# Kernel tuning notes

Measured on AMD Instinct MI355X. Metric: run time of the kernel, lower is better.

The kernel has to match this reference:

```python
import jax, jax.numpy as jnp
import numpy as np

BAND_WIDTH = 0.05
EPS = 1e-5
NORM_EPS = 1e-12  # F.normalize clamp_min


def _l2_normalize_channels(x):
    # x: (B, C, D, H, W); normalize over channel dim=1 like F.normalize(p=2, dim=1)
    n = jnp.sqrt(jnp.sum(x * x, axis=1, keepdims=True))
    return x / jnp.maximum(n, NORM_EPS)


def setup_inputs() -> dict:
    key = jax.random.key(0)
    k1, k2, k3 = jax.random.split(key, 3)
    B, C, D, H, W = 2, 256, 8, 8, 8
    P, K = 128, 512  # n_patches iterations, k=512 sampled voxels per patch
    S = D * H * W  # 512 spatial voxels
    t2_feat = jax.random.normal(k1, (B, C, D, H, W), dtype=jnp.float32)
    t1_feat = jax.random.normal(k2, (B, C, D, H, W), dtype=jnp.float32)
    idx = jax.random.randint(k3, (P, K), 0, S, dtype=jnp.int32)
    return {"t2_feat": t2_feat, "t1_feat": t1_feat, "idx": idx}


def reference(t2_feat, t1_feat, idx):
    B, C = t2_feat.shape[:2]
    # normalize channels, flatten spatial dims: (B, C, S)
    t2 = _l2_normalize_channels(t2_feat).reshape(B, C, -1)
    t1 = _l2_normalize_channels(t1_feat).reshape(B, C, -1)
    # gather the same random voxels for both modalities: (B, C, P, K)
    t2p = t2[:, :, idx]
    t1p = t1[:, :, idx]
    # batched cosine similarity: bmm(t2p^T, t1p) per patch -> (P, B, K, K)
    cs = jnp.einsum('bcpk,bcpl->pbkl', t2p, t1p)
    e = jnp.exp(cs / BAND_WIDTH)
    pos = jnp.diagonal(e, axis1=2, axis2=3)  # (P, B, K) exp of positives
    # InfoNCE over columns (torch dim=1 of (B,K,K)) and rows (dim=2)
    info_nce1 = pos / jnp.sum(e, axis=2)
    info_nce2 = pos / jnp.sum(e, axis=3)
    info_nce = 0.5 * (info_nce1 + info_nce2)
    # per-patch mean of -log, then mean over patches == global mean
    return jnp.mean(-jnp.log(info_nce + EPS))
```

## Files before the change

### kernel.cpp

```cpp
#include <hip/hip_runtime.h>

typedef __attribute__((ext_vector_type(8))) short bf16x8;
typedef __attribute__((ext_vector_type(4))) float f32x4;
typedef __attribute__((ext_vector_type(4))) ushort u16x4;

#define C_DIM 256
#define S_DIM 512
#define P_DIM 128
#define K_DIM 512
#define INV_BW 20.0f
#define EPS_LOSS 1e-5f

#define OFF_SS2    0
#define OFF_SS1    1024
#define OFF_DIAG   2048
#define OFF_CNTBF  3072
#define OFF_T2BF   35840
#define OFF_T1BF   166912
#define OFF_EBF    297984
#define OFF_ETBF   560128
#define OFF_D1     822272
#define OFF_D2     1084416
#define OFF_PART   1346560
#define OFF_BAR    1346816

__device__ inline ushort f2bf(float f) {
  union { float f; uint u; } v; v.f = f;
  return (ushort)((v.u + 0x7FFF + ((v.u >> 16) & 1)) >> 16);
}

#define TP 260
__global__ __launch_bounds__(256) void pre_kernel(
    const float* __restrict__ t2, const float* __restrict__ t1,
    const int* __restrict__ idx,
    float* __restrict__ ss2, float* __restrict__ ss1,
    ushort* __restrict__ t2bfT, ushort* __restrict__ t1bfT,
    ushort* __restrict__ cntbf, int* __restrict__ bar) {
  int blk = blockIdx.x, tid = threadIdx.x;
  if (blk < 128) {
    __shared__ ushort tl[16][TP];
    __shared__ float ps[16][17];
    int tt = blk >> 6, b = (blk >> 5) & 1, stile = blk & 31;
    int s0 = stile * 16;
    const float* src = (tt ? t1 : t2) + b * (C_DIM * S_DIM);
    ushort* dst = (tt ? t1bfT : t2bfT) + b * (S_DIM * C_DIM);
    float* ssd = (tt ? ss1 : ss2) + b * S_DIM;
    int ls = tid & 15, cg = tid >> 4;
    float a = 0.f;
    #pragma unroll
    for (int k = 0; k < 16; ++k) {
      int c = cg + 16 * k;
      float v = src[c * S_DIM + s0 + ls];
      a += v * v;
      tl[ls][c] = f2bf(v);
    }
    ps[cg][ls] = a;
    __syncthreads();
    if (tid < 16) {
      float ss = 0.f;
      #pragma unroll
      for (int j = 0; j < 16; ++j) ss += ps[j][tid];
      ssd[s0 + tid] = ss;
    }
    int wv = tid >> 6, ln = tid & 63;
    #pragma unroll
    for (int i = 0; i < 4; ++i) {
      int sl = wv * 4 + i;
      u16x4 pk = *reinterpret_cast<const u16x4*>(&tl[sl][ln * 4]);
      *reinterpret_cast<u16x4*>(&dst[(s0 + sl) * C_DIM + ln * 4]) = pk;
    }
  } else {
    __shared__ int c_lds[S_DIM];
    int p = blk - 128;
    if (blk == 128 && tid < 3) bar[tid] = 0;
    c_lds[tid] = 0; c_lds[tid + 256] = 0;
    __syncthreads();
    atomicAdd(&c_lds[idx[p * K_DIM + tid]], 1);
    atomicAdd(&c_lds[idx[p * K_DIM + tid + 256]], 1);
    __syncthreads();
    cntbf[p * S_DIM + tid]       = f2bf((float)c_lds[tid]);
    cntbf[p * S_DIM + tid + 256] = f2bf((float)c_lds[tid + 256]);
  }
}

__global__ __launch_bounds__(256) void gemm_exp_mfma_kernel(
    const ushort* __restrict__ t2bfT, const ushort* __restrict__ t1bfT,
    const float* __restrict__ ss2, const float* __restrict__ ss1,
    ushort* __restrict__ Ebf, ushort* __restrict__ ETbf,
    float* __restrict__ diag) {
  int wave = threadIdx.x >> 6, lane = threadIdx.x & 63;
  int job = blockIdx.x * 4 + wave;
  int n = job & 31, mp = (job >> 5) & 15, b = job >> 9;
  int c0 = n * 16;
  int lr = lane & 15, lo = lane >> 4;
  const ushort* base2 = t2bfT + b * (S_DIM * C_DIM);
  const ushort* bp = t1bfT + b * (S_DIM * C_DIM) + (c0 + lr) * C_DIM + lo * 8;
  bf16x8 bfr[8];
  #pragma unroll
  for (int k = 0; k < 8; ++k)
    bfr[k] = *reinterpret_cast<const bf16x8*>(bp + k * 32);
  float bs = 1.0f / fmaxf(sqrtf(ss1[b * S_DIM + c0 + lr]), 1e-12f);
  ushort* Eb  = Ebf  + b * (S_DIM * S_DIM);
  ushort* ETb = ETbf + b * (S_DIM * S_DIM);
  #pragma unroll
  for (int t = 0; t < 2; ++t) {
    int m0 = mp * 32 + t * 16;
    const ushort* ap = base2 + (m0 + lr) * C_DIM + lo * 8;
    f32x4 acc = {0.f, 0.f, 0.f, 0.f};
    #pragma unroll
    for (int k = 0; k < 8; ++k) {
      bf16x8 af = *reinterpret_cast<const bf16x8*>(ap + k * 32);
      acc = __builtin_amdgcn_mfma_f32_16x16x32_bf16(af, bfr[k], acc, 0, 0, 0);
    }
    float e[4]; ushort eb[4];
    #pragma unroll
    for (int r = 0; r < 4; ++r) {
      int row = m0 + lo * 4 + r;
      float as = 1.0f / fmaxf(sqrtf(ss2[b * S_DIM + row]), 1e-12f);
      e[r] = __expf(acc[r] * as * bs * INV_BW);
      eb[r] = f2bf(e[r]);
      Eb[row * S_DIM + c0 + lr] = eb[r];
    }
    u16x4 pk = {eb[0], eb[1], eb[2], eb[3]};
    *reinterpret_cast<u16x4*>(&ETb[(c0 + lr) * S_DIM + m0 + lo * 4]) = pk;
    if (m0 == c0 && (lr >> 2) == lo) diag[b * S_DIM + m0 + lr] = e[lr & 3];
  }
}

__global__ __launch_bounds__(256) void denom_mfma_kernel(
    const ushort* __restrict__ Ebf, const ushort* __restrict__ ETbf,
    const ushort* __restrict__ cntbf,
    float* __restrict__ D1, float* __restrict__ D2) {
  int wave = threadIdx.x >> 6, lane = threadIdx.x & 63;
  int job = blockIdx.x * 4 + wave;
  int np = job & 15, m = (job >> 4) & 7, b = (job >> 7) & 1;
  int z = (job >> 8) & 1, h = job >> 9;
  int m0 = m * 16;
  int lr = lane & 15, lo = lane >> 4;
  const ushort* Bmat = (z ? Ebf : ETbf) + b * (S_DIM * S_DIM);
  float* Dp = (z ? D2 : D1);
  const ushort* aptr = cntbf + (m0 + lr) * S_DIM + h * 256 + lo * 8;
  bf16x8 afr[8];
  #pragma unroll
  for (int k = 0; k < 8; ++k)
    afr[k] = *reinterpret_cast<const bf16x8*>(aptr + k * 32);
  #pragma unroll
  for (int t = 0; t < 2; ++t) {
    int col0 = np * 32 + t * 16;
    const ushort* bptr = Bmat + (col0 + lr) * S_DIM + h * 256 + lo * 8;
    f32x4 acc = {0.f, 0.f, 0.f, 0.f};
    #pragma unroll
    for (int k = 0; k < 8; ++k) {
      bf16x8 bv = *reinterpret_cast<const bf16x8*>(bptr + k * 32);
      acc = __builtin_amdgcn_mfma_f32_16x16x32_bf16(afr[k], bv, acc, 0, 0, 0);
    }
    #pragma unroll
    for (int r = 0; r < 4; ++r) {
      int p = m0 + lo * 4 + r;
      Dp[((h * P_DIM + p) * 2 + b) * S_DIM + col0 + lr] = acc[r];
    }
  }
}

__global__ __launch_bounds__(512) void loss_final_kernel(
    const int* __restrict__ idx, const float* __restrict__ diag,
    const float* __restrict__ D1, const float* __restrict__ D2,
    float* __restrict__ part, int* __restrict__ bar, float* __restrict__ out) {
  const int HOFF = P_DIM * 2 * S_DIM;
  int p = blockIdx.x, k = threadIdx.x;
  int s = idx[p * K_DIM + k];
  float acc = 0.f;
  #pragma unroll
  for (int b = 0; b < 2; ++b) {
    float pos = diag[b * S_DIM + s];
    int o = (p * 2 + b) * S_DIM + s;
    float d1 = D1[o] + D1[HOFF + o];
    float d2 = D2[o] + D2[HOFF + o];
    acc += __logf(0.5f * (pos / d1 + pos / d2) + EPS_LOSS);
  }
  for (int o = 32; o; o >>= 1) acc += __shfl_down(acc, o);
  __shared__ float red[8];
  __shared__ int lastflag;
  if ((k & 63) == 0) red[k >> 6] = acc;
  __syncthreads();
  if (k == 0) {
    float tsum = 0.f;
    #pragma unroll
    for (int i = 0; i < 8; ++i) tsum += red[i];
    atomicExch(&part[p], tsum);
    __threadfence();
    int old = atomicAdd(&bar[2], 1);
    lastflag = (old == P_DIM - 1);
  }
  __syncthreads();
  if (lastflag) {
    __threadfence();
    float v = (k < P_DIM) ? atomicAdd(&part[k], 0.0f) : 0.0f;
    for (int o = 32; o; o >>= 1) v += __shfl_down(v, o);
    __shared__ float red2[8];
    if ((k & 63) == 0) red2[k >> 6] = v;
    __syncthreads();
    if (k == 0) {
      float tsum = 0.f;
      #pragma unroll
      for (int i = 0; i < 8; ++i) tsum += red2[i];
      out[0] = -tsum * (1.0f / (P_DIM * 2.0f * K_DIM));
    }
  }
}

extern "C" void kernel_launch(void* const* d_in, const int* in_sizes, int n_in,
                              void* d_out, int out_size, void* d_ws, size_t ws_size,
                              hipStream_t stream) {
  const float* t2 = (const float*)d_in[0];
  const float* t1 = (const float*)d_in[1];
  const int* idx  = (const int*)d_in[2];
  float* ws = (float*)d_ws;
  float*  ss2    = ws + OFF_SS2;
  float*  ss1    = ws + OFF_SS1;
  float*  diag   = ws + OFF_DIAG;
  ushort* cntbf  = (ushort*)(ws + OFF_CNTBF);
  ushort* t2bfT  = (ushort*)(ws + OFF_T2BF);
  ushort* t1bfT  = (ushort*)(ws + OFF_T1BF);
  ushort* Ebf    = (ushort*)(ws + OFF_EBF);
  ushort* ETbf   = (ushort*)(ws + OFF_ETBF);
  float*  D1     = ws + OFF_D1;
  float*  D2     = ws + OFF_D2;
  float*  part   = ws + OFF_PART;
  int*    bar    = (int*)(ws + OFF_BAR);

  pre_kernel<<<256, 256, 0, stream>>>(t2, t1, idx, ss2, ss1, t2bfT, t1bfT,
                                      cntbf, bar);
  gemm_exp_mfma_kernel<<<256, 256, 0, stream>>>(t2bfT, t1bfT, ss2, ss1,
                                                Ebf, ETbf, diag);
  denom_mfma_kernel<<<256, 256, 0, stream>>>(Ebf, ETbf, cntbf, D1, D2);
  loss_final_kernel<<<P_DIM, 512, 0, stream>>>(idx, diag, D1, D2, part, bar,
                                               (float*)d_out);
}
```

Before: 30.08 us.

## Fuse preprocessing into gram-exp and histogram kernels, drop a launch

Removes the separate preprocessing kernel. The gram/exp kernel now loads fp32 features directly, converts them to bf16 in LDS and computes channel norms locally. Each 32x32 tile re-reads its input slice, which adds redundant global reads in exchange for one fewer launch and no transposed intermediate buffers. The denominator kernel builds per-patch voxel histograms in LDS from idx and runs the full K=512 reduction per block, so the split-K halves and their summation in the loss kernel go away. The catch is that every block recomputes its histograms, duplicating that atomic work.

```diff
diff --git a/kernel.cpp b/kernel.cpp
--- a/kernel.cpp
+++ b/kernel.cpp
@@ -11,154 +11,133 @@
 #define INV_BW 20.0f
 #define EPS_LOSS 1e-5f
 
-#define OFF_SS2    0
-#define OFF_SS1    1024
-#define OFF_DIAG   2048
-#define OFF_CNTBF  3072
-#define OFF_T2BF   35840
-#define OFF_T1BF   166912
-#define OFF_EBF    297984
-#define OFF_ETBF   560128
-#define OFF_D1     822272
-#define OFF_D2     1084416
-#define OFF_PART   1346560
-#define OFF_BAR    1346816
+#define OFF_DIAG   0
+#define OFF_EBF    1024
+#define OFF_ETBF   263168
+#define OFF_D1     525312
+#define OFF_D2     656384
+#define OFF_PART   787456
+#define OFF_BAR    787584
 
 __device__ inline ushort f2bf(float f) {
   union { float f; uint u; } v; v.f = f;
   return (ushort)((v.u + 0x7FFF + ((v.u >> 16) & 1)) >> 16);
 }
-
-#define TP 260
-__global__ __launch_bounds__(256) void pre_kernel(
+__device__ inline float bf2f(ushort u) {
+  union { uint u; float f; } v; v.u = ((uint)u) << 16;
+  return v.f;
+}
+
+__global__ __launch_bounds__(256) void gram_exp_kernel(
     const float* __restrict__ t2, const float* __restrict__ t1,
-    const int* __restrict__ idx,
-    float* __restrict__ ss2, float* __restrict__ ss1,
-    ushort* __restrict__ t2bfT, ushort* __restrict__ t1bfT,
-    ushort* __restrict__ cntbf, int* __restrict__ bar) {
+    ushort* __restrict__ Ebf, ushort* __restrict__ ETbf,
+    float* __restrict__ diag, int* __restrict__ bar) {
+  __shared__ ushort A_[32][264];
+  __shared__ ushort B_[32][264];
+  __shared__ float sA[32], sB[32];
   int blk = blockIdx.x, tid = threadIdx.x;
-  if (blk < 128) {
-    __shared__ ushort tl[16][TP];
-    __shared__ float ps[16][17];
-    int tt = blk >> 6, b = (blk >> 5) & 1, stile = blk & 31;
-    int s0 = stile * 16;
-    const float* src = (tt ? t1 : t2) + b * (C_DIM * S_DIM);
-    ushort* dst = (tt ? t1bfT : t2bfT) + b * (S_DIM * C_DIM);
-    float* ssd = (tt ? ss1 : ss2) + b * S_DIM;
-    int ls = tid & 15, cg = tid >> 4;
-    float a = 0.f;
-    #pragma unroll
-    for (int k = 0; k < 16; ++k) {
-      int c = cg + 16 * k;
-      float v = src[c * S_DIM + s0 + ls];
-      a += v * v;
-      tl[ls][c] = f2bf(v);
-    }
-    ps[cg][ls] = a;
-    __syncthreads();
-    if (tid < 16) {
-      float ss = 0.f;
-      #pragma unroll
-      for (int j = 0; j < 16; ++j) ss += ps[j][tid];
-      ssd[s0 + tid] = ss;
-    }
-    int wv = tid >> 6, ln = tid & 63;
-    #pragma unroll
-    for (int i = 0; i < 4; ++i) {
-      int sl = wv * 4 + i;
-      u16x4 pk = *reinterpret_cast<const u16x4*>(&tl[sl][ln * 4]);
-      *reinterpret_cast<u16x4*>(&dst[(s0 + sl) * C_DIM + ln * 4]) = pk;
-    }
-  } else {
-    __shared__ int c_lds[S_DIM];
-    int p = blk - 128;
-    if (blk == 128 && tid < 3) bar[tid] = 0;
-    c_lds[tid] = 0; c_lds[tid + 256] = 0;
-    __syncthreads();
-    atomicAdd(&c_lds[idx[p * K_DIM + tid]], 1);
-    atomicAdd(&c_lds[idx[p * K_DIM + tid + 256]], 1);
-    __syncthreads();
-    cntbf[p * S_DIM + tid]       = f2bf((float)c_lds[tid]);
-    cntbf[p * S_DIM + tid + 256] = f2bf((float)c_lds[tid + 256]);
-  }
-}
-
-__global__ __launch_bounds__(256) void gemm_exp_mfma_kernel(
-    const ushort* __restrict__ t2bfT, const ushort* __restrict__ t1bfT,
-    const float* __restrict__ ss2, const float* __restrict__ ss1,
-    ushort* __restrict__ Ebf, ushort* __restrict__ ETbf,
-    float* __restrict__ diag) {
-  int wave = threadIdx.x >> 6, lane = threadIdx.x & 63;
-  int job = blockIdx.x * 4 + wave;
-  int n = job & 31, mp = (job >> 5) & 15, b = job >> 9;
-  int c0 = n * 16;
+  if (blk == 0 && tid == 0) bar[0] = 0;
+  int mb = blk & 15, nb = (blk >> 4) & 15, b = blk >> 8;
+  int m0 = mb * 32, c0 = nb * 32;
+  {
+    const float* pa = t2 + (b * C_DIM + tid) * S_DIM + m0;
+    const float* pb = t1 + (b * C_DIM + tid) * S_DIM + c0;
+    #pragma unroll
+    for (int q = 0; q < 8; ++q) {
+      float4 va = *reinterpret_cast<const float4*>(pa + q * 4);
+      float4 vb = *reinterpret_cast<const float4*>(pb + q * 4);
+      A_[q * 4 + 0][tid] = f2bf(va.x); A_[q * 4 + 1][tid] = f2bf(va.y);
+      A_[q * 4 + 2][tid] = f2bf(va.z); A_[q * 4 + 3][tid] = f2bf(va.w);
+      B_[q * 4 + 0][tid] = f2bf(vb.x); B_[q * 4 + 1][tid] = f2bf(vb.y);
+      B_[q * 4 + 2][tid] = f2bf(vb.z); B_[q * 4 + 3][tid] = f2bf(vb.w);
+    }
+  }
+  __syncthreads();
+  if (tid < 64) {
+    const ushort* row = (tid < 32) ? &A_[tid][0] : &B_[tid - 32][0];
+    float a0 = 0.f, a1 = 0.f, a2 = 0.f, a3 = 0.f;
+    #pragma unroll
+    for (int k = 0; k < 64; ++k) {
+      u16x4 v = *reinterpret_cast<const u16x4*>(row + k * 4);
+      float x0 = bf2f(v.x), x1 = bf2f(v.y), x2 = bf2f(v.z), x3 = bf2f(v.w);
+      a0 += x0 * x0; a1 += x1 * x1; a2 += x2 * x2; a3 += x3 * x3;
+    }
+    float sc = 1.0f / fmaxf(sqrtf((a0 + a1) + (a2 + a3)), 1e-12f);
+    if (tid < 32) sA[tid] = sc; else sB[tid - 32] = sc;
+  }
+  __syncthreads();
+  int wave = tid >> 6, lane = tid & 63;
+  int tm = wave & 1, tn = wave >> 1;
   int lr = lane & 15, lo = lane >> 4;
-  const ushort* base2 = t2bfT + b * (S_DIM * C_DIM);
-  const ushort* bp = t1bfT + b * (S_DIM * C_DIM) + (c0 + lr) * C_DIM + lo * 8;
-  bf16x8 bfr[8];
-  #pragma unroll
-  for (int k = 0; k < 8; ++k)
-    bfr[k] = *reinterpret_cast<const bf16x8*>(bp + k * 32);
-  float bs = 1.0f / fmaxf(sqrtf(ss1[b * S_DIM + c0 + lr]), 1e-12f);
+  f32x4 acc = {0.f, 0.f, 0.f, 0.f};
+  #pragma unroll
+  for (int k = 0; k < 8; ++k) {
+    bf16x8 af = *reinterpret_cast<const bf16x8*>(&A_[tm * 16 + lr][lo * 8 + k * 32]);
+    bf16x8 bv = *reinterpret_cast<const bf16x8*>(&B_[tn * 16 + lr][lo * 8 + k * 32]);
+    acc = __builtin_amdgcn_mfma_f32_16x16x32_bf16(af, bv, acc, 0, 0, 0);
+  }
+  int mg0 = m0 + tm * 16, cg0 = c0 + tn * 16;
+  float bs = sB[tn * 16 + lr];
   ushort* Eb  = Ebf  + b * (S_DIM * S_DIM);
   ushort* ETb = ETbf + b * (S_DIM * S_DIM);
-  #pragma unroll
-  for (int t = 0; t < 2; ++t) {
-    int m0 = mp * 32 + t * 16;
-    const ushort* ap = base2 + (m0 + lr) * C_DIM + lo * 8;
-    f32x4 acc = {0.f, 0.f, 0.f, 0.f};
-    #pragma unroll
-    for (int k = 0; k < 8; ++k) {
-      bf16x8 af = *reinterpret_cast<const bf16x8*>(ap + k * 32);
-      acc = __builtin_amdgcn_mfma_f32_16x16x32_bf16(af, bfr[k], acc, 0, 0, 0);
-    }
-    float e[4]; ushort eb[4];
-    #pragma unroll
-    for (int r = 0; r < 4; ++r) {
-      int row = m0 + lo * 4 + r;
-      float as = 1.0f / fmaxf(sqrtf(ss2[b * S_DIM + row]), 1e-12f);
-      e[r] = __expf(acc[r] * as * bs * INV_BW);
-      eb[r] = f2bf(e[r]);
-      Eb[row * S_DIM + c0 + lr] = eb[r];
-    }
-    u16x4 pk = {eb[0], eb[1], eb[2], eb[3]};
-    *reinterpret_cast<u16x4*>(&ETb[(c0 + lr) * S_DIM + m0 + lo * 4]) = pk;
-    if (m0 == c0 && (lr >> 2) == lo) diag[b * S_DIM + m0 + lr] = e[lr & 3];
-  }
-}
-
-__global__ __launch_bounds__(256) void denom_mfma_kernel(
+  float e[4]; ushort eb[4];
+  #pragma unroll
+  for (int r = 0; r < 4; ++r) {
+    int rl = tm * 16 + lo * 4 + r;
+    float ev = __expf(acc[r] * sA[rl] * bs * INV_BW);
+    e[r] = ev; eb[r] = f2bf(ev);
+    Eb[(m0 + rl) * S_DIM + cg0 + lr] = eb[r];
+  }
+  u16x4 pk = {eb[0], eb[1], eb[2], eb[3]};
+  *reinterpret_cast<u16x4*>(&ETb[(cg0 + lr) * S_DIM + mg0 + lo * 4]) = pk;
+  if (mg0 == cg0 && (lr >> 2) == lo) diag[b * S_DIM + mg0 + lr] = e[lr & 3];
+}
+
+__global__ __launch_bounds__(256) void denom_kernel(
     const ushort* __restrict__ Ebf, const ushort* __restrict__ ETbf,
-    const ushort* __restrict__ cntbf,
+    const int* __restrict__ idx,
     float* __restrict__ D1, float* __restrict__ D2) {
-  int wave = threadIdx.x >> 6, lane = threadIdx.x & 63;
-  int job = blockIdx.x * 4 + wave;
-  int np = job & 15, m = (job >> 4) & 7, b = (job >> 7) & 1;
-  int z = (job >> 8) & 1, h = job >> 9;
-  int m0 = m * 16;
+  __shared__ int hist[16][516];
+  __shared__ ushort cb[16][520];
+  int blk = blockIdx.x, tid = threadIdx.x;
+  int m = blk & 7, ng = (blk >> 3) & 7, b = (blk >> 6) & 1, z = blk >> 7;
+  int p0 = m * 16;
+  #pragma unroll
+  for (int i = 0; i < 32; ++i) hist[(tid * 32 + i) >> 9][(tid * 32 + i) & 511] = 0;
+  __syncthreads();
+  {
+    int p = tid >> 4, l16 = tid & 15;
+    const int* ip = idx + (p0 + p) * K_DIM + l16;
+    #pragma unroll
+    for (int j = 0; j < 32; ++j) atomicAdd(&hist[p][ip[j * 16]], 1);
+  }
+  __syncthreads();
+  {
+    int p = tid >> 4, l16 = tid & 15;
+    #pragma unroll
+    for (int j = 0; j < 32; ++j) {
+      int col = l16 + j * 16;
+      cb[p][col] = f2bf((float)hist[p][col]);
+    }
+  }
+  __syncthreads();
+  int wave = tid >> 6, lane = tid & 63;
   int lr = lane & 15, lo = lane >> 4;
+  int col0 = (ng * 4 + wave) * 16;
   const ushort* Bmat = (z ? Ebf : ETbf) + b * (S_DIM * S_DIM);
-  float* Dp = (z ? D2 : D1);
-  const ushort* aptr = cntbf + (m0 + lr) * S_DIM + h * 256 + lo * 8;
-  bf16x8 afr[8];
-  #pragma unroll
-  for (int k = 0; k < 8; ++k)
-    afr[k] = *reinterpret_cast<const bf16x8*>(aptr + k * 32);
-  #pragma unroll
-  for (int t = 0; t < 2; ++t) {
-    int col0 = np * 32 + t * 16;
-    const ushort* bptr = Bmat + (col0 + lr) * S_DIM + h * 256 + lo * 8;
-    f32x4 acc = {0.f, 0.f, 0.f, 0.f};
-    #pragma unroll
-    for (int k = 0; k < 8; ++k) {
-      bf16x8 bv = *reinterpret_cast<const bf16x8*>(bptr + k * 32);
-      acc = __builtin_amdgcn_mfma_f32_16x16x32_bf16(afr[k], bv, acc, 0, 0, 0);
-    }
-    #pragma unroll
-    for (int r = 0; r < 4; ++r) {
-      int p = m0 + lo * 4 + r;
-      Dp[((h * P_DIM + p) * 2 + b) * S_DIM + col0 + lr] = acc[r];
-    }
+  const ushort* bptr = Bmat + (col0 + lr) * S_DIM + lo * 8;
+  f32x4 acc = {0.f, 0.f, 0.f, 0.f};
+  #pragma unroll
+  for (int k = 0; k < 16; ++k) {
+    bf16x8 af = *reinterpret_cast<const bf16x8*>(&cb[lr][lo * 8 + k * 32]);
+    bf16x8 bv = *reinterpret_cast<const bf16x8*>(bptr + k * 32);
+    acc = __builtin_amdgcn_mfma_f32_16x16x32_bf16(af, bv, acc, 0, 0, 0);
+  }
+  float* Dp = z ? D2 : D1;
+  #pragma unroll
+  for (int r = 0; r < 4; ++r) {
+    int p = p0 + lo * 4 + r;
+    Dp[(p * 2 + b) * S_DIM + col0 + lr] = acc[r];
   }
 }
 
@@ -166,7 +145,6 @@
     const int* __restrict__ idx, const float* __restrict__ diag,
     const float* __restrict__ D1, const float* __restrict__ D2,
     float* __restrict__ part, int* __restrict__ bar, float* __restrict__ out) {
-  const int HOFF = P_DIM * 2 * S_DIM;
   int p = blockIdx.x, k = threadIdx.x;
   int s = idx[p * K_DIM + k];
   float acc = 0.f;
@@ -174,8 +152,8 @@
   for (int b = 0; b < 2; ++b) {
     float pos = diag[b * S_DIM + s];
     int o = (p * 2 + b) * S_DIM + s;
-    float d1 = D1[o] + D1[HOFF + o];
-    float d2 = D2[o] + D2[HOFF + o];
+    float d1 = D1[o];
+    float d2 = D2[o];
     acc += __logf(0.5f * (pos / d1 + pos / d2) + EPS_LOSS);
   }
   for (int o = 32; o; o >>= 1) acc += __shfl_down(acc, o);
@@ -189,7 +167,7 @@
     for (int i = 0; i < 8; ++i) tsum += red[i];
     atomicExch(&part[p], tsum);
     __threadfence();
-    int old = atomicAdd(&bar[2], 1);
+    int old = atomicAdd(&bar[0], 1);
     lastflag = (old == P_DIM - 1);
   }
   __syncthreads();
@@ -216,12 +194,7 @@
   const float* t1 = (const float*)d_in[1];
   const int* idx  = (const int*)d_in[2];
   float* ws = (float*)d_ws;
-  float*  ss2    = ws + OFF_SS2;
-  float*  ss1    = ws + OFF_SS1;
   float*  diag   = ws + OFF_DIAG;
-  ushort* cntbf  = (ushort*)(ws + OFF_CNTBF);
-  ushort* t2bfT  = (ushort*)(ws + OFF_T2BF);
-  ushort* t1bfT  = (ushort*)(ws + OFF_T1BF);
   ushort* Ebf    = (ushort*)(ws + OFF_EBF);
   ushort* ETbf   = (ushort*)(ws + OFF_ETBF);
   float*  D1     = ws + OFF_D1;
@@ -229,11 +202,8 @@
   float*  part   = ws + OFF_PART;
   int*    bar    = (int*)(ws + OFF_BAR);
 
-  pre_kernel<<<256, 256, 0, stream>>>(t2, t1, idx, ss2, ss1, t2bfT, t1bfT,
-                                      cntbf, bar);
-  gemm_exp_mfma_kernel<<<256, 256, 0, stream>>>(t2bfT, t1bfT, ss2, ss1,
-                                                Ebf, ETbf, diag);
-  denom_mfma_kernel<<<256, 256, 0, stream>>>(Ebf, ETbf, cntbf, D1, D2);
+  gram_exp_kernel<<<512, 256, 0, stream>>>(t2, t1, Ebf, ETbf, diag, bar);
+  denom_kernel<<<256, 256, 0, stream>>>(Ebf, ETbf, idx, D1, D2);
   loss_final_kernel<<<P_DIM, 512, 0, stream>>>(idx, diag, D1, D2, part, bar,
                                                (float*)d_out);
 }
```

Result: faster. 29.37 us (-2.4%).
